# Kernel tuning notes

Measured on AMD Instinct MI355X. Metric: run time of the kernel, lower is better.

The kernel has to match this reference:

```python
import jax, jax.numpy as jnp
import numpy as np

BETA = 0.25
EMA_DECAY = 0.99
EMA_EPS = 1e-05
K = 8192
D = 512


def setup_inputs() -> dict:
    key = jax.random.key(0)
    k1, k2, k3, k4 = jax.random.split(key, 4)
    z = jax.random.normal(k1, (8, 2048, D), dtype=jnp.float32)
    codebook_weight = jax.random.normal(k2, (K, D), dtype=jnp.float32)
    ema_cluster_size = jax.random.uniform(k3, (K,), dtype=jnp.float32)
    ema_embed_avg = jax.random.normal(k4, (K, D), dtype=jnp.float32)
    return {"z": z, "codebook_weight": codebook_weight,
            "ema_cluster_size": ema_cluster_size, "ema_embed_avg": ema_embed_avg}


def reference(z, codebook_weight, ema_cluster_size, ema_embed_avg):
    d = z.shape[-1]
    flat = z.reshape(-1, d)                                  # [N, D]
    z_sq = jnp.sum(flat * flat, axis=1, keepdims=True)       # [N, 1]
    e = codebook_weight                                      # [K, D]
    e_sq = jnp.sum(e * e, axis=1)                            # [K]
    # logits = -||z - e||^2 (argmax over logits == nearest code)
    logits = -(z_sq - 2.0 * jnp.matmul(flat, e.T) + e_sq)    # [N, K]
    idx = jnp.argmax(logits, axis=1)                         # [N]
    z_q = e[idx].reshape(z.shape)

    # commitment loss: beta * sum((z - sg[z_q])^2) / D
    vq_loss = BETA * jnp.sum((z - jax.lax.stop_gradient(z_q)) ** 2) / d

    # EMA statistics (torch.no_grad block)
    flat_sg = jax.lax.stop_gradient(flat)
    n_codes = e.shape[0]
    ones = jnp.ones(flat.shape[0], dtype=flat.dtype)
    cluster_size = jax.ops.segment_sum(ones, idx, num_segments=n_codes)       # == onehot.sum(0)
    embed_sum = jax.ops.segment_sum(flat_sg, idx, num_segments=n_codes)       # == onehot.T @ flat
    new_ema_cluster_size = ema_cluster_size * EMA_DECAY + cluster_size * (1.0 - EMA_DECAY)
    new_ema_embed_avg = ema_embed_avg * EMA_DECAY + embed_sum * (1.0 - EMA_DECAY)
    updated = new_ema_embed_avg / (new_ema_cluster_size[:, None] + EMA_EPS)
    active = (cluster_size > 0)[:, None]
    new_codebook = jnp.where(active, updated, codebook_weight)
    # (random reseeding of never-used codes is intentionally omitted: it is
    # nondeterministic and outside the deterministic math path)

    # straight-through estimator
    z_out = z + jax.lax.stop_gradient(z_q - z)
    return (z_out, vq_loss, new_ema_cluster_size, new_ema_embed_avg, new_codebook)
```

## Files before the change

kernel.cpp:

```cpp
#include <hip/hip_runtime.h>
#include <hip/hip_bf16.h>

#define N_ROWS 16384
#define DDIM   512
#define KCODES 8192
#define BETA   0.25f
#define DECAY  0.99f
#define ONE_MINUS_DECAY 0.01f
#define EMA_EPS 1e-5f

#define O_Z    0
#define O_LOSS 8388608
#define O_CS   8388609
#define O_AVG  8396801
#define O_CB   12591105

#define WS_CNT      0
#define WS_ESQ      32768
#define WS_FLAGCNT  65536
#define WS_FLAGLIST 65792
#define WS_KEYS     73984
#define WS_TBK      205056
#define WS_TSD      4399360
#define WS_Z16      6496512
#define WS_CB16     23273728

#define TAU  0.35f
#define RCAP 2048

typedef _Float16 half8  __attribute__((ext_vector_type(8)));
typedef float    floatx4 __attribute__((ext_vector_type(4)));

__device__ __forceinline__ unsigned enc_f(float d) {
    unsigned ub = __float_as_uint(d);
    return (ub & 0x80000000u) ? ~ub : (ub | 0x80000000u);
}
__device__ __forceinline__ float dec_key(unsigned long long k) {
    unsigned ub = (unsigned)(k >> 32);
    ub = (ub & 0x80000000u) ? (ub ^ 0x80000000u) : ~ub;
    return __uint_as_float(ub);
}

__device__ __forceinline__ float4 pack8_f16(float4 a, float4 b) {
    auto p0 = __builtin_amdgcn_cvt_pkrtz(a.x, a.y);
    auto p1 = __builtin_amdgcn_cvt_pkrtz(a.z, a.w);
    auto p2 = __builtin_amdgcn_cvt_pkrtz(b.x, b.y);
    auto p3 = __builtin_amdgcn_cvt_pkrtz(b.z, b.w);
    float4 r;
    r.x = __builtin_bit_cast(float, p0);
    r.y = __builtin_bit_cast(float, p1);
    r.z = __builtin_bit_cast(float, p2);
    r.w = __builtin_bit_cast(float, p3);
    return r;
}

__device__ __forceinline__ void load_lds16(const void* g, void* l) {
    __builtin_amdgcn_global_load_lds(
        (const __attribute__((address_space(1))) unsigned int*)g,
        (__attribute__((address_space(3))) unsigned int*)l, 16, 0, 0);
}

__global__ __launch_bounds__(256) void cvtz_kernel(const float* __restrict__ z,
                                                   _Float16* __restrict__ z16) {
    size_t i = (size_t)blockIdx.x * 256 + threadIdx.x;
    const float4* p = (const float4*)z + 2 * i;
    ((float4*)z16)[i] = pack8_f16(p[0], p[1]);
}

__global__ __launch_bounds__(64) void cvtcb_kernel(const float* __restrict__ cb,
                                                   _Float16* __restrict__ cb16,
                                                   float* __restrict__ e_sq) {
    int k = blockIdx.x;
    int t = threadIdx.x;
    const float4* r = (const float4*)(cb + (size_t)k * DDIM);
    float4 a = r[2 * t], b = r[2 * t + 1];
    ((float4*)(cb16 + (size_t)k * DDIM))[t] = pack8_f16(a, b);
    float s = a.x*a.x + a.y*a.y + a.z*a.z + a.w*a.w
            + b.x*b.x + b.y*b.y + b.z*b.z + b.w*b.w;
    #pragma unroll
    for (int o = 32; o > 0; o >>= 1) s += __shfl_down(s, o);
    if (t == 0) e_sq[k] = s;
}

__global__ void prepass_kernel(const float* __restrict__ ema_cs,
                               const float* __restrict__ ema_avg,
                               float* __restrict__ out) {
    int i = blockIdx.x * 256 + threadIdx.x;
    if (i < KCODES * DDIM) out[O_AVG + i] = DECAY * ema_avg[i];
    if (i < KCODES)        out[O_CS + i]  = DECAY * ema_cs[i];
    if (i == 0)            out[O_LOSS]    = 0.0f;
}

__global__ __launch_bounds__(256, 2) void screen_kernel(
    const _Float16* __restrict__ z16, const _Float16* __restrict__ cb16,
    const float* __restrict__ e_sq,
    unsigned long long* __restrict__ tbk, float* __restrict__ tsd) {
    __shared__ _Float16 zt[128 * 64];
    __shared__ _Float16 ct[256 * 64];
    __shared__ float eb_d1[2][128];
    __shared__ int   eb_c1[2][128];
    __shared__ float eb_d2[2][128];

    const int tid = threadIdx.x;
    const int bx = blockIdx.x;
    const int by = blockIdx.y;
    const int lane = tid & 63, wid = tid >> 6;
    const int wm = wid & 1, wn = wid >> 1;
    const int lr = lane & 15, lq = lane >> 4;

    const _Float16* zsrc[4]; _Float16* zdst[4];
    #pragma unroll
    for (int r = 0; r < 4; r++) {
        int g = (r * 4 + wid) * 64 + lane;
        int row = g >> 3, kq = g & 7;
        zsrc[r] = z16 + (size_t)(by * 128 + row) * DDIM + ((kq ^ (row & 7)) << 3);
        zdst[r] = &zt[(r * 4 + wid) * 512];
    }
    const _Float16* csrc[8]; _Float16* cdst[8];
    #pragma unroll
    for (int r = 0; r < 8; r++) {
        int g = (r * 4 + wid) * 64 + lane;
        int row = g >> 3, kq = g & 7;
        csrc[r] = cb16 + (size_t)(bx * 256 + row) * DDIM + ((kq ^ (row & 7)) << 3);
        cdst[r] = &ct[(r * 4 + wid) * 512];
    }

    floatx4 acc[4][8];
    #pragma unroll
    for (int i = 0; i < 4; i++)
        #pragma unroll
        for (int j = 0; j < 8; j++) acc[i][j] = floatx4{0.f, 0.f, 0.f, 0.f};

    for (int kc = 0; kc < DDIM; kc += 64) {
        #pragma unroll
        for (int r = 0; r < 4; r++) load_lds16(zsrc[r] + kc, zdst[r]);
        #pragma unroll
        for (int r = 0; r < 8; r++) load_lds16(csrc[r] + kc, cdst[r]);
        __syncthreads();
        #pragma unroll
        for (int kk = 0; kk < 2; kk++) {
            half8 av[4];
            #pragma unroll
            for (int mt = 0; mt < 4; mt++) {
                int row = wm * 64 + mt * 16 + lr;
                av[mt] = *(const half8*)&zt[row * 64 + (((kk * 4 + lq) ^ (row & 7)) << 3)];
            }
            #pragma unroll
            for (int nt = 0; nt < 8; nt++) {
                int row = wn * 128 + nt * 16 + lr;
                half8 bv = *(const half8*)&ct[row * 64 + (((kk * 4 + lq) ^ (row & 7)) << 3)];
                #pragma unroll
                for (int mt = 0; mt < 4; mt++)
                    acc[mt][nt] = __builtin_amdgcn_mfma_f32_16x16x32_f16(av[mt], bv, acc[mt][nt], 0, 0, 0);
            }
        }
        __syncthreads();
    }

    float es[8];
    #pragma unroll
    for (int nt = 0; nt < 8; nt++) es[nt] = e_sq[bx * 256 + wn * 128 + nt * 16 + lr];

    #pragma unroll
    for (int mt = 0; mt < 4; mt++) {
        #pragma unroll
        for (int r = 0; r < 4; r++) {
            float d1 = 1e30f, d2 = 1e30f; int c1 = 0x7FFFFFFF;
            #pragma unroll
            for (int nt = 0; nt < 8; nt++) {
                float d = fmaf(-2.0f, acc[mt][nt][r], es[nt]);
                int c = bx * 256 + wn * 128 + nt * 16 + lr;
                bool better = (d < d1) || (d == d1 && c < c1);
                if (better) { d2 = d1; d1 = d; c1 = c; }
                else        { d2 = fminf(d2, d); }
            }
            #pragma unroll
            for (int off = 1; off < 16; off <<= 1) {
                float od1 = __shfl_xor(d1, off);
                int   oc1 = __shfl_xor(c1, off);
                float od2 = __shfl_xor(d2, off);
                bool better = (od1 < d1) || (od1 == d1 && oc1 < c1);
                if (better) { d2 = fminf(d1, od2); d1 = od1; c1 = oc1; }
                else        { d2 = fminf(d2, od1); }
            }
            if (lr == 0) {
                int row = wm * 64 + mt * 16 + lq * 4 + r;
                eb_d1[wn][row] = d1; eb_c1[wn][row] = c1; eb_d2[wn][row] = d2;
            }
        }
    }
    __syncthreads();
    if (tid < 128) {
        float d1a = eb_d1[0][tid], d2a = eb_d2[0][tid]; int c1a = eb_c1[0][tid];
        float d1b = eb_d1[1][tid], d2b = eb_d2[1][tid]; int c1b = eb_c1[1][tid];
        bool bbet = (d1b < d1a) || (d1b == d1a && c1b < c1a);
        float d1 = bbet ? d1b : d1a; int c1 = bbet ? c1b : c1a;
        float d2 = bbet ? fminf(d1a, d2b) : fminf(d2a, d1b);
        unsigned long long key = ((unsigned long long)enc_f(d1) << 32) | (unsigned)c1;
        int row_g = by * 128 + tid;
        tbk[(size_t)row_g * 32 + bx] = key;
        tsd[(size_t)row_g * 32 + bx] = d2;
    }
}

__global__ void merge_kernel(const unsigned long long* __restrict__ tbk,
                             const float* __restrict__ tsd,
                             unsigned long long* __restrict__ keys,
                             int* __restrict__ flagcnt, int* __restrict__ flaglist) {
    int row = blockIdx.x * 256 + threadIdx.x;
    const unsigned long long* t = tbk + (size_t)row * 32;
    const float* s = tsd + (size_t)row * 32;
    unsigned long long kb = t[0];
    float sec = s[0];
    for (int i = 1; i < 32; i++) {
        unsigned long long k = t[i]; float s2 = s[i];
        if (k < kb) { sec = fminf(fminf(sec, s2), dec_key(kb)); kb = k; }
        else        { sec = fminf(sec, fminf(s2, dec_key(k))); }
    }
    float best = dec_key(kb);
    if (sec - best < TAU) {
        int pos = atomicAdd(flagcnt, 1);
        if (pos < RCAP) { flaglist[pos] = row; keys[row] = ~0ULL; }
        else keys[row] = kb;
    } else {
        keys[row] = kb;
    }
}

__global__ __launch_bounds__(256) void rescore_kernel(
    const float* __restrict__ z, const float* __restrict__ cb,
    const float* __restrict__ e_sq, const int* __restrict__ flagcnt,
    const int* __restrict__ flaglist, unsigned long long* __restrict__ keys) {
    int n = *flagcnt; n = min(n, RCAP);
    int base = blockIdx.y * 32;
    if (base >= n) return;
    __shared__ float ech[128][65];
    __shared__ float zch[32][65];
    __shared__ int ridx[32];
    __shared__ unsigned long long redk[32][33];
    const int tid = threadIdx.x;
    const int bx = blockIdx.x;
    if (tid < 32) ridx[tid] = flaglist[min(base + tid, n - 1)];
    __syncthreads();
    const int tc = tid & 31, tg = tid >> 5;
    float acc[4][4] = {};
    for (int kc = 0; kc < DDIM; kc += 64) {
        #pragma unroll
        for (int l = 0; l < 8; l++) {
            int idx = tid + 256 * l;
            int row = idx >> 4, q = idx & 15;
            float4 v = *(const float4*)&cb[(size_t)(bx * 128 + row) * DDIM + kc + q * 4];
            ech[row][q*4+0] = v.x; ech[row][q*4+1] = v.y; ech[row][q*4+2] = v.z; ech[row][q*4+3] = v.w;
        }
        #pragma unroll
        for (int l = 0; l < 2; l++) {
            int idx = tid + 256 * l;
            int row = idx >> 4, q = idx & 15;
            float4 v = *(const float4*)&z[(size_t)ridx[row] * DDIM + kc + q * 4];
            zch[row][q*4+0] = v.x; zch[row][q*4+1] = v.y; zch[row][q*4+2] = v.z; zch[row][q*4+3] = v.w;
        }
        __syncthreads();
        for (int k = 0; k < 64; k++) {
            float a0 = zch[tg*4+0][k], a1 = zch[tg*4+1][k], a2 = zch[tg*4+2][k], a3 = zch[tg*4+3][k];
            float b0 = ech[tc*4+0][k], b1 = ech[tc*4+1][k], b2 = ech[tc*4+2][k], b3 = ech[tc*4+3][k];
            acc[0][0] = fmaf(a0,b0,acc[0][0]); acc[0][1] = fmaf(a0,b1,acc[0][1]);
            acc[0][2] = fmaf(a0,b2,acc[0][2]); acc[0][3] = fmaf(a0,b3,acc[0][3]);
            acc[1][0] = fmaf(a1,b0,acc[1][0]); acc[1][1] = fmaf(a1,b1,acc[1][1]);
            acc[1][2] = fmaf(a1,b2,acc[1][2]); acc[1][3] = fmaf(a1,b3,acc[1][3]);
            acc[2][0] = fmaf(a2,b0,acc[2][0]); acc[2][1] = fmaf(a2,b1,acc[2][1]);
            acc[2][2] = fmaf(a2,b2,acc[2][2]); acc[2][3] = fmaf(a2,b3,acc[2][3]);
            acc[3][0] = fmaf(a3,b0,acc[3][0]); acc[3][1] = fmaf(a3,b1,acc[3][1]);
            acc[3][2] = fmaf(a3,b2,acc[3][2]); acc[3][3] = fmaf(a3,b3,acc[3][3]);
        }
        __syncthreads();
    }
    #pragma unroll
    for (int i = 0; i < 4; i++) {
        unsigned long long bk = ~0ULL;
        #pragma unroll
        for (int j = 0; j < 4; j++) {
            int code = bx * 128 + tc * 4 + j;
            float d = fmaf(-2.0f, acc[i][j], e_sq[code]);
            unsigned long long key = ((unsigned long long)enc_f(d) << 32) | (unsigned)code;
            bk = (key < bk) ? key : bk;
        }
        redk[tg * 4 + i][tc] = bk;
    }
    __syncthreads();
    if (tid < 32) {
        unsigned long long b = redk[tid][0];
        #pragma unroll
        for (int t = 1; t < 32; t++) {
            unsigned long long v = redk[tid][t];
            b = (v < b) ? v : b;
        }
        atomicMin(&keys[ridx[tid]], b);
    }
}

__global__ __launch_bounds__(128) void gather_stats_kernel(
    const float* __restrict__ z, const float* __restrict__ cb,
    const unsigned long long* __restrict__ keys,
    float* __restrict__ out, float* __restrict__ cnt) {
    const int row = blockIdx.x;
    const int tid = threadIdx.x;
    const int idx = (int)(unsigned int)(keys[row] & 0xFFFFFFFFull);

    const float4 zv = ((const float4*)(z  + (size_t)row * DDIM))[tid];
    const float4 ev = ((const float4*)(cb + (size_t)idx * DDIM))[tid];
    ((float4*)(out + O_Z + (size_t)row * DDIM))[tid] = ev;

    float dx = zv.x - ev.x, dy = zv.y - ev.y, dz = zv.z - ev.z, dw = zv.w - ev.w;
    float s = dx*dx + dy*dy + dz*dz + dw*dw;

    float* o3 = out + O_AVG + (size_t)idx * DDIM + tid * 4;
    atomicAdd(o3 + 0, ONE_MINUS_DECAY * zv.x);
    atomicAdd(o3 + 1, ONE_MINUS_DECAY * zv.y);
    atomicAdd(o3 + 2, ONE_MINUS_DECAY * zv.z);
    atomicAdd(o3 + 3, ONE_MINUS_DECAY * zv.w);

    #pragma unroll
    for (int o = 32; o > 0; o >>= 1) s += __shfl_down(s, o);
    __shared__ float red[2];
    if ((tid & 63) == 0) red[tid >> 6] = s;
    __syncthreads();
    if (tid == 0) {
        atomicAdd(out + O_LOSS, (red[0] + red[1]) * (BETA / (float)DDIM));
        atomicAdd(&cnt[idx], 1.0f);
        atomicAdd(out + O_CS + idx, ONE_MINUS_DECAY);
    }
}

__global__ void finalize_kernel(const float* __restrict__ cb,
                                const float* __restrict__ cnt,
                                float* __restrict__ out) {
    int i = blockIdx.x * 256 + threadIdx.x;
    if (i >= KCODES * DDIM) return;
    int k = i >> 9;
    float avg = out[O_AVG + i];
    float ncs = out[O_CS + k];
    float upd = avg / (ncs + EMA_EPS);
    out[O_CB + i] = (cnt[k] > 0.0f) ? upd : cb[i];
}

extern "C" void kernel_launch(void* const* d_in, const int* in_sizes, int n_in,
                              void* d_out, int out_size, void* d_ws, size_t ws_size,
                              hipStream_t stream) {
    const float* z       = (const float*)d_in[0];
    const float* cb      = (const float*)d_in[1];
    const float* ema_cs  = (const float*)d_in[2];
    const float* ema_avg = (const float*)d_in[3];
    float* out = (float*)d_out;

    float* cnt  = (float*)((char*)d_ws + WS_CNT);
    float* e_sq = (float*)((char*)d_ws + WS_ESQ);
    int* flagcnt = (int*)((char*)d_ws + WS_FLAGCNT);
    int* flaglist = (int*)((char*)d_ws + WS_FLAGLIST);
    unsigned long long* keys = (unsigned long long*)((char*)d_ws + WS_KEYS);
    unsigned long long* tbk = (unsigned long long*)((char*)d_ws + WS_TBK);
    float* tsd = (float*)((char*)d_ws + WS_TSD);
    _Float16* z16  = (_Float16*)((char*)d_ws + WS_Z16);
    _Float16* cb16 = (_Float16*)((char*)d_ws + WS_CB16);

    hipMemsetAsync(cnt, 0, KCODES * sizeof(float), stream);
    hipMemsetAsync(flagcnt, 0, sizeof(int), stream);

    cvtz_kernel<<<N_ROWS * DDIM / 8 / 256, 256, 0, stream>>>(z, z16);
    cvtcb_kernel<<<KCODES, 64, 0, stream>>>(cb, cb16, e_sq);
    prepass_kernel<<<(KCODES * DDIM + 255) / 256, 256, 0, stream>>>(ema_cs, ema_avg, out);
    screen_kernel<<<dim3(KCODES / 256, N_ROWS / 128), 256, 0, stream>>>(z16, cb16, e_sq, tbk, tsd);
    merge_kernel<<<N_ROWS / 256, 256, 0, stream>>>(tbk, tsd, keys, flagcnt, flaglist);
    rescore_kernel<<<dim3(KCODES / 128, RCAP / 32), 256, 0, stream>>>(z, cb, e_sq, flagcnt, flaglist, keys);
    gather_stats_kernel<<<N_ROWS, 128, 0, stream>>>(z, cb, keys, out, cnt);
    finalize_kernel<<<(KCODES * DDIM + 255) / 256, 256, 0, stream>>>(cb, cnt, out);
}
```

Baseline: 731.2 us.

## Replace atomic EMA scatter with sorted row lists and shrink screen tiles

The screen kernel now uses 128x128 tiles with higher occupancy and merges per-tile best/second-best distances directly into per-row keys with atomicMin, removing the tile buffers and most of the merge pass. The float atomic scatter into ema_embed_avg plus the separate prepass and finalize kernels are replaced by count, prefix scan, row-list fill and a per-code gather kernel that fuses the EMA and codebook update. The loss goes through 64 partial sums. This trades many contended atomics for extra small launches, including a single-block scan. Summation order changes, so results may differ slightly.

```diff
diff --git a/kernel.cpp b/kernel.cpp
--- a/kernel.cpp
+++ b/kernel.cpp
@@ -20,10 +20,14 @@
 #define WS_FLAGCNT  65536
 #define WS_FLAGLIST 65792
 #define WS_KEYS     73984
-#define WS_TBK      205056
-#define WS_TSD      4399360
-#define WS_Z16      6496512
-#define WS_CB16     23273728
+#define WS_SEC2     205056
+#define WS_LOSSP    270592
+#define WS_IDXS     270848
+#define WS_OFFS     336384
+#define WS_CURS     369152
+#define WS_ROWLIST  401920
+#define WS_Z16      467456
+#define WS_CB16     17244672
 
 #define TAU  0.35f
 #define RCAP 2048
@@ -35,10 +39,11 @@
     unsigned ub = __float_as_uint(d);
     return (ub & 0x80000000u) ? ~ub : (ub | 0x80000000u);
 }
+__device__ __forceinline__ float dec32(unsigned ub) {
+    return __uint_as_float((ub & 0x80000000u) ? (ub ^ 0x80000000u) : ~ub);
+}
 __device__ __forceinline__ float dec_key(unsigned long long k) {
-    unsigned ub = (unsigned)(k >> 32);
-    ub = (ub & 0x80000000u) ? (ub ^ 0x80000000u) : ~ub;
-    return __uint_as_float(ub);
+    return dec32((unsigned)(k >> 32));
 }
 
 __device__ __forceinline__ float4 pack8_f16(float4 a, float4 b) {
@@ -82,60 +87,40 @@
     if (t == 0) e_sq[k] = s;
 }
 
-__global__ void prepass_kernel(const float* __restrict__ ema_cs,
-                               const float* __restrict__ ema_avg,
-                               float* __restrict__ out) {
-    int i = blockIdx.x * 256 + threadIdx.x;
-    if (i < KCODES * DDIM) out[O_AVG + i] = DECAY * ema_avg[i];
-    if (i < KCODES)        out[O_CS + i]  = DECAY * ema_cs[i];
-    if (i == 0)            out[O_LOSS]    = 0.0f;
-}
-
-__global__ __launch_bounds__(256, 2) void screen_kernel(
+__global__ __launch_bounds__(256, 4) void screen_kernel(
     const _Float16* __restrict__ z16, const _Float16* __restrict__ cb16,
     const float* __restrict__ e_sq,
-    unsigned long long* __restrict__ tbk, float* __restrict__ tsd) {
+    unsigned long long* __restrict__ keys, unsigned* __restrict__ sec2) {
     __shared__ _Float16 zt[128 * 64];
-    __shared__ _Float16 ct[256 * 64];
-    __shared__ float eb_d1[2][128];
-    __shared__ int   eb_c1[2][128];
-    __shared__ float eb_d2[2][128];
+    __shared__ _Float16 ct[128 * 64];
 
     const int tid = threadIdx.x;
-    const int bx = blockIdx.x;
-    const int by = blockIdx.y;
+    const int by = blockIdx.x;
+    const int bx = blockIdx.y;
     const int lane = tid & 63, wid = tid >> 6;
     const int wm = wid & 1, wn = wid >> 1;
     const int lr = lane & 15, lq = lane >> 4;
 
-    const _Float16* zsrc[4]; _Float16* zdst[4];
+    const _Float16* zsrc[4]; const _Float16* csrc[4];
     #pragma unroll
     for (int r = 0; r < 4; r++) {
         int g = (r * 4 + wid) * 64 + lane;
         int row = g >> 3, kq = g & 7;
         zsrc[r] = z16 + (size_t)(by * 128 + row) * DDIM + ((kq ^ (row & 7)) << 3);
-        zdst[r] = &zt[(r * 4 + wid) * 512];
-    }
-    const _Float16* csrc[8]; _Float16* cdst[8];
-    #pragma unroll
-    for (int r = 0; r < 8; r++) {
-        int g = (r * 4 + wid) * 64 + lane;
-        int row = g >> 3, kq = g & 7;
-        csrc[r] = cb16 + (size_t)(bx * 256 + row) * DDIM + ((kq ^ (row & 7)) << 3);
-        cdst[r] = &ct[(r * 4 + wid) * 512];
-    }
-
-    floatx4 acc[4][8];
+        csrc[r] = cb16 + (size_t)(bx * 128 + row) * DDIM + ((kq ^ (row & 7)) << 3);
+    }
+
+    floatx4 acc[4][4];
     #pragma unroll
     for (int i = 0; i < 4; i++)
         #pragma unroll
-        for (int j = 0; j < 8; j++) acc[i][j] = floatx4{0.f, 0.f, 0.f, 0.f};
+        for (int j = 0; j < 4; j++) acc[i][j] = floatx4{0.f, 0.f, 0.f, 0.f};
 
     for (int kc = 0; kc < DDIM; kc += 64) {
         #pragma unroll
-        for (int r = 0; r < 4; r++) load_lds16(zsrc[r] + kc, zdst[r]);
-        #pragma unroll
-        for (int r = 0; r < 8; r++) load_lds16(csrc[r] + kc, cdst[r]);
+        for (int r = 0; r < 4; r++) load_lds16(zsrc[r] + kc, &zt[(r * 4 + wid) * 512]);
+        #pragma unroll
+        for (int r = 0; r < 4; r++) load_lds16(csrc[r] + kc, &ct[(r * 4 + wid) * 512]);
         __syncthreads();
         #pragma unroll
         for (int kk = 0; kk < 2; kk++) {
@@ -146,8 +131,8 @@
                 av[mt] = *(const half8*)&zt[row * 64 + (((kk * 4 + lq) ^ (row & 7)) << 3)];
             }
             #pragma unroll
-            for (int nt = 0; nt < 8; nt++) {
-                int row = wn * 128 + nt * 16 + lr;
+            for (int nt = 0; nt < 4; nt++) {
+                int row = wn * 64 + nt * 16 + lr;
                 half8 bv = *(const half8*)&ct[row * 64 + (((kk * 4 + lq) ^ (row & 7)) << 3)];
                 #pragma unroll
                 for (int mt = 0; mt < 4; mt++)
@@ -157,9 +142,13 @@
         __syncthreads();
     }
 
-    float es[8];
-    #pragma unroll
-    for (int nt = 0; nt < 8; nt++) es[nt] = e_sq[bx * 256 + wn * 128 + nt * 16 + lr];
+    float* eb_d1 = (float*)zt;
+    int*   eb_c1 = (int*)zt + 256;
+    float* eb_d2 = (float*)zt + 512;
+
+    float es[4];
+    #pragma unroll
+    for (int nt = 0; nt < 4; nt++) es[nt] = e_sq[bx * 128 + wn * 64 + nt * 16 + lr];
 
     #pragma unroll
     for (int mt = 0; mt < 4; mt++) {
@@ -167,9 +156,9 @@
         for (int r = 0; r < 4; r++) {
             float d1 = 1e30f, d2 = 1e30f; int c1 = 0x7FFFFFFF;
             #pragma unroll
-            for (int nt = 0; nt < 8; nt++) {
+            for (int nt = 0; nt < 4; nt++) {
                 float d = fmaf(-2.0f, acc[mt][nt][r], es[nt]);
-                int c = bx * 256 + wn * 128 + nt * 16 + lr;
+                int c = bx * 128 + wn * 64 + nt * 16 + lr;
                 bool better = (d < d1) || (d == d1 && c < c1);
                 if (better) { d2 = d1; d1 = d; c1 = c; }
                 else        { d2 = fminf(d2, d); }
@@ -185,45 +174,35 @@
             }
             if (lr == 0) {
                 int row = wm * 64 + mt * 16 + lq * 4 + r;
-                eb_d1[wn][row] = d1; eb_c1[wn][row] = c1; eb_d2[wn][row] = d2;
+                eb_d1[wn * 128 + row] = d1; eb_c1[wn * 128 + row] = c1; eb_d2[wn * 128 + row] = d2;
             }
         }
     }
     __syncthreads();
     if (tid < 128) {
-        float d1a = eb_d1[0][tid], d2a = eb_d2[0][tid]; int c1a = eb_c1[0][tid];
-        float d1b = eb_d1[1][tid], d2b = eb_d2[1][tid]; int c1b = eb_c1[1][tid];
+        float d1a = eb_d1[tid],       d2a = eb_d2[tid];       int c1a = eb_c1[tid];
+        float d1b = eb_d1[128 + tid], d2b = eb_d2[128 + tid]; int c1b = eb_c1[128 + tid];
         bool bbet = (d1b < d1a) || (d1b == d1a && c1b < c1a);
         float d1 = bbet ? d1b : d1a; int c1 = bbet ? c1b : c1a;
         float d2 = bbet ? fminf(d1a, d2b) : fminf(d2a, d1b);
         unsigned long long key = ((unsigned long long)enc_f(d1) << 32) | (unsigned)c1;
         int row_g = by * 128 + tid;
-        tbk[(size_t)row_g * 32 + bx] = key;
-        tsd[(size_t)row_g * 32 + bx] = d2;
-    }
-}
-
-__global__ void merge_kernel(const unsigned long long* __restrict__ tbk,
-                             const float* __restrict__ tsd,
-                             unsigned long long* __restrict__ keys,
+        unsigned long long old = atomicMin(&keys[row_g], key);
+        float cand = (key < old) ? fminf(dec_key(old), d2) : fminf(d1, d2);
+        atomicMin(&sec2[row_g], enc_f(cand));
+    }
+}
+
+__global__ void merge_kernel(unsigned long long* __restrict__ keys,
+                             const unsigned* __restrict__ sec2,
                              int* __restrict__ flagcnt, int* __restrict__ flaglist) {
     int row = blockIdx.x * 256 + threadIdx.x;
-    const unsigned long long* t = tbk + (size_t)row * 32;
-    const float* s = tsd + (size_t)row * 32;
-    unsigned long long kb = t[0];
-    float sec = s[0];
-    for (int i = 1; i < 32; i++) {
-        unsigned long long k = t[i]; float s2 = s[i];
-        if (k < kb) { sec = fminf(fminf(sec, s2), dec_key(kb)); kb = k; }
-        else        { sec = fminf(sec, fminf(s2, dec_key(k))); }
-    }
+    unsigned long long kb = keys[row];
     float best = dec_key(kb);
+    float sec  = dec32(sec2[row]);
     if (sec - best < TAU) {
         int pos = atomicAdd(flagcnt, 1);
         if (pos < RCAP) { flaglist[pos] = row; keys[row] = ~0ULL; }
-        else keys[row] = kb;
-    } else {
-        keys[row] = kb;
     }
 }
 
@@ -298,10 +277,11 @@
     }
 }
 
-__global__ __launch_bounds__(128) void gather_stats_kernel(
+__global__ __launch_bounds__(128) void zout_loss_kernel(
     const float* __restrict__ z, const float* __restrict__ cb,
     const unsigned long long* __restrict__ keys,
-    float* __restrict__ out, float* __restrict__ cnt) {
+    float* __restrict__ out, int* __restrict__ cnt,
+    int* __restrict__ idxs, float* __restrict__ lossp) {
     const int row = blockIdx.x;
     const int tid = threadIdx.x;
     const int idx = (int)(unsigned int)(keys[row] & 0xFFFFFFFFull);
@@ -312,12 +292,6 @@
 
     float dx = zv.x - ev.x, dy = zv.y - ev.y, dz = zv.z - ev.z, dw = zv.w - ev.w;
     float s = dx*dx + dy*dy + dz*dz + dw*dw;
-
-    float* o3 = out + O_AVG + (size_t)idx * DDIM + tid * 4;
-    atomicAdd(o3 + 0, ONE_MINUS_DECAY * zv.x);
-    atomicAdd(o3 + 1, ONE_MINUS_DECAY * zv.y);
-    atomicAdd(o3 + 2, ONE_MINUS_DECAY * zv.z);
-    atomicAdd(o3 + 3, ONE_MINUS_DECAY * zv.w);
 
     #pragma unroll
     for (int o = 32; o > 0; o >>= 1) s += __shfl_down(s, o);
@@ -325,22 +299,91 @@
     if ((tid & 63) == 0) red[tid >> 6] = s;
     __syncthreads();
     if (tid == 0) {
-        atomicAdd(out + O_LOSS, (red[0] + red[1]) * (BETA / (float)DDIM));
-        atomicAdd(&cnt[idx], 1.0f);
-        atomicAdd(out + O_CS + idx, ONE_MINUS_DECAY);
-    }
-}
-
-__global__ void finalize_kernel(const float* __restrict__ cb,
-                                const float* __restrict__ cnt,
-                                float* __restrict__ out) {
-    int i = blockIdx.x * 256 + threadIdx.x;
-    if (i >= KCODES * DDIM) return;
-    int k = i >> 9;
-    float avg = out[O_AVG + i];
-    float ncs = out[O_CS + k];
-    float upd = avg / (ncs + EMA_EPS);
-    out[O_CB + i] = (cnt[k] > 0.0f) ? upd : cb[i];
+        atomicAdd(&lossp[row & 63], red[0] + red[1]);
+        atomicAdd(&cnt[idx], 1);
+        idxs[row] = idx;
+    }
+}
+
+__global__ void loss_final_kernel(const float* __restrict__ lossp, float* __restrict__ out) {
+    float s = lossp[threadIdx.x];
+    #pragma unroll
+    for (int o = 32; o > 0; o >>= 1) s += __shfl_down(s, o);
+    if (threadIdx.x == 0) out[O_LOSS] = s * (BETA / (float)DDIM);
+}
+
+__global__ __launch_bounds__(256) void scan_kernel(
+    const int* __restrict__ cnt, const float* __restrict__ ema_cs,
+    float* __restrict__ out, int* __restrict__ offs, int* __restrict__ curs) {
+    __shared__ int tot[256];
+    const int t = threadIdx.x;
+    const int base = t * 32;
+    int local[32]; int s = 0;
+    #pragma unroll
+    for (int j = 0; j < 32; j++) { local[j] = cnt[base + j]; s += local[j]; }
+    tot[t] = s;
+    __syncthreads();
+    for (int off = 1; off < 256; off <<= 1) {
+        int v = (t >= off) ? tot[t - off] : 0;
+        __syncthreads();
+        tot[t] += v;
+        __syncthreads();
+    }
+    int run = tot[t] - s;
+    #pragma unroll
+    for (int j = 0; j < 32; j++) {
+        offs[base + j] = run; curs[base + j] = run;
+        out[O_CS + base + j] = DECAY * ema_cs[base + j] + ONE_MINUS_DECAY * (float)local[j];
+        run += local[j];
+    }
+}
+
+__global__ void fill_kernel(const int* __restrict__ idxs, int* __restrict__ curs,
+                            int* __restrict__ rowlist) {
+    int row = blockIdx.x * 256 + threadIdx.x;
+    int idx = idxs[row];
+    int pos = atomicAdd(&curs[idx], 1);
+    rowlist[pos] = row;
+}
+
+__global__ __launch_bounds__(256) void code_update_kernel(
+    const float* __restrict__ z, const float* __restrict__ cb,
+    const float* __restrict__ ema_cs, const float* __restrict__ ema_avg,
+    const int* __restrict__ cnt, const int* __restrict__ offs,
+    const int* __restrict__ rowlist, float* __restrict__ out) {
+    const int lane = threadIdx.x & 63;
+    const int k = blockIdx.x * 4 + (threadIdx.x >> 6);
+    const int n = cnt[k], off = offs[k];
+    float4 a0 = {0.f,0.f,0.f,0.f}, a1 = {0.f,0.f,0.f,0.f};
+    for (int r = 0; r < n; r++) {
+        int row = rowlist[off + r];
+        const float4* zp = (const float4*)(z + (size_t)row * DDIM) + lane * 2;
+        float4 v0 = zp[0], v1 = zp[1];
+        a0.x += v0.x; a0.y += v0.y; a0.z += v0.z; a0.w += v0.w;
+        a1.x += v1.x; a1.y += v1.y; a1.z += v1.z; a1.w += v1.w;
+    }
+    const float4* ep = (const float4*)(ema_avg + (size_t)k * DDIM) + lane * 2;
+    float4 e0 = ep[0], e1 = ep[1];
+    float4 n0, n1;
+    n0.x = DECAY * e0.x + ONE_MINUS_DECAY * a0.x; n0.y = DECAY * e0.y + ONE_MINUS_DECAY * a0.y;
+    n0.z = DECAY * e0.z + ONE_MINUS_DECAY * a0.z; n0.w = DECAY * e0.w + ONE_MINUS_DECAY * a0.w;
+    n1.x = DECAY * e1.x + ONE_MINUS_DECAY * a1.x; n1.y = DECAY * e1.y + ONE_MINUS_DECAY * a1.y;
+    n1.z = DECAY * e1.z + ONE_MINUS_DECAY * a1.z; n1.w = DECAY * e1.w + ONE_MINUS_DECAY * a1.w;
+    ((float4*)(out + O_AVG + (size_t)k * DDIM))[lane * 2]     = n0;
+    ((float4*)(out + O_AVG + (size_t)k * DDIM))[lane * 2 + 1] = n1;
+
+    float ncs = DECAY * ema_cs[k] + ONE_MINUS_DECAY * (float)n;
+    float inv = 1.0f / (ncs + EMA_EPS);
+    float4 c0, c1;
+    if (n > 0) {
+        c0.x = n0.x * inv; c0.y = n0.y * inv; c0.z = n0.z * inv; c0.w = n0.w * inv;
+        c1.x = n1.x * inv; c1.y = n1.y * inv; c1.z = n1.z * inv; c1.w = n1.w * inv;
+    } else {
+        const float4* cp = (const float4*)(cb + (size_t)k * DDIM) + lane * 2;
+        c0 = cp[0]; c1 = cp[1];
+    }
+    ((float4*)(out + O_CB + (size_t)k * DDIM))[lane * 2]     = c0;
+    ((float4*)(out + O_CB + (size_t)k * DDIM))[lane * 2 + 1] = c1;
 }
 
 extern "C" void kernel_launch(void* const* d_in, const int* in_sizes, int n_in,
@@ -352,25 +395,34 @@
     const float* ema_avg = (const float*)d_in[3];
     float* out = (float*)d_out;
 
-    float* cnt  = (float*)((char*)d_ws + WS_CNT);
-    float* e_sq = (float*)((char*)d_ws + WS_ESQ);
-    int* flagcnt = (int*)((char*)d_ws + WS_FLAGCNT);
-    int* flaglist = (int*)((char*)d_ws + WS_FLAGLIST);
+    int* cnt       = (int*)((char*)d_ws + WS_CNT);
+    float* e_sq    = (float*)((char*)d_ws + WS_ESQ);
+    int* flagcnt   = (int*)((char*)d_ws + WS_FLAGCNT);
+    int* flaglist  = (int*)((char*)d_ws + WS_FLAGLIST);
     unsigned long long* keys = (unsigned long long*)((char*)d_ws + WS_KEYS);
-    unsigned long long* tbk = (unsigned long long*)((char*)d_ws + WS_TBK);
-    float* tsd = (float*)((char*)d_ws + WS_TSD);
+    unsigned* sec2 = (unsigned*)((char*)d_ws + WS_SEC2);
+    float* lossp   = (float*)((char*)d_ws + WS_LOSSP);
+    int* idxs      = (int*)((char*)d_ws + WS_IDXS);
+    int* offs      = (int*)((char*)d_ws + WS_OFFS);
+    int* curs      = (int*)((char*)d_ws + WS_CURS);
+    int* rowlist   = (int*)((char*)d_ws + WS_ROWLIST);
     _Float16* z16  = (_Float16*)((char*)d_ws + WS_Z16);
     _Float16* cb16 = (_Float16*)((char*)d_ws + WS_CB16);
 
-    hipMemsetAsync(cnt, 0, KCODES * sizeof(float), stream);
+    hipMemsetAsync(cnt, 0, KCODES * sizeof(int), stream);
     hipMemsetAsync(flagcnt, 0, sizeof(int), stream);
+    hipMemsetAsync(keys, 0xFF, N_ROWS * sizeof(unsigned long long), stream);
+    hipMemsetAsync(sec2, 0xFF, N_ROWS * sizeof(unsigned), stream);
+    hipMemsetAsync(lossp, 0, 64 * sizeof(float), stream);
 
     cvtz_kernel<<<N_ROWS * DDIM / 8 / 256, 256, 0, stream>>>(z, z16);
     cvtcb_kernel<<<KCODES, 64, 0, stream>>>(cb, cb16, e_sq);
-    prepass_kernel<<<(KCODES * DDIM + 255) / 256, 256, 0, stream>>>(ema_cs, ema_avg, out);
-    screen_kernel<<<dim3(KCODES / 256, N_ROWS / 128), 256, 0, stream>>>(z16, cb16, e_sq, tbk, tsd);
-    merge_kernel<<<N_ROWS / 256, 256, 0, stream>>>(tbk, tsd, keys, flagcnt, flaglist);
+    screen_kernel<<<dim3(N_ROWS / 128, KCODES / 128), 256, 0, stream>>>(z16, cb16, e_sq, keys, sec2);
+    merge_kernel<<<N_ROWS / 256, 256, 0, stream>>>(keys, sec2, flagcnt, flaglist);
     rescore_kernel<<<dim3(KCODES / 128, RCAP / 32), 256, 0, stream>>>(z, cb, e_sq, flagcnt, flaglist, keys);
-    gather_stats_kernel<<<N_ROWS, 128, 0, stream>>>(z, cb, keys, out, cnt);
-    finalize_kernel<<<(KCODES * DDIM + 255) / 256, 256, 0, stream>>>(cb, cnt, out);
-}
+    zout_loss_kernel<<<N_ROWS, 128, 0, stream>>>(z, cb, keys, out, cnt, idxs, lossp);
+    loss_final_kernel<<<1, 64, 0, stream>>>(lossp, out);
+    scan_kernel<<<1, 256, 0, stream>>>(cnt, ema_cs, out, offs, curs);
+    fill_kernel<<<N_ROWS / 256, 256, 0, stream>>>(idxs, curs, rowlist);
+    code_update_kernel<<<KCODES / 4, 256, 0, stream>>>(z, cb, ema_cs, ema_avg, cnt, offs, rowlist, out);
+}
```

Measured after the change: 646.8 us. 1.13x faster.
